# Optimization experiments

Measured on AMD Instinct MI355X. Metric: run time of the kernel, lower is better.

## Reference

```python
import jax, jax.numpy as jnp
import numpy as np

N, F = 1024, 512
H, W = 128, 128
TANX = TANY = 0.5
SCALE_MOD = 1.0


def quat_to_rot(q):
    q = q / jnp.linalg.norm(q, axis=-1, keepdims=True)
    r, x, y, z = q[:, 0], q[:, 1], q[:, 2], q[:, 3]
    R = jnp.stack([
        1 - 2 * (y * y + z * z), 2 * (x * y - r * z), 2 * (x * z + r * y),
        2 * (x * y + r * z), 1 - 2 * (x * x + z * z), 2 * (y * z - r * x),
        2 * (x * z - r * y), 2 * (y * z + r * x), 1 - 2 * (x * x + y * y)], -1)
    return R.reshape(-1, 3, 3)


def setup_inputs() -> dict:
    key = jax.random.key(0)
    ks = jax.random.split(key, 9)
    u = jax.random.uniform(ks[0], (N, 3))
    # place gaussians in front of the camera (z in [2,6], x/y within frustum)
    means3D = jnp.stack([(u[:, 0] - 0.5) * 2.0, (u[:, 1] - 0.5) * 2.0,
                         2.0 + 4.0 * u[:, 2]], axis=1)
    means2D = jnp.zeros((N, 3), jnp.float32)  # grad holder, unused in fwd math
    opacities = 0.05 + 0.9 * jax.random.uniform(ks[1], (N, 1))
    colors_precomp = jax.random.uniform(ks[2], (N, 3))
    semantic_feature = jax.random.uniform(ks[3], (N, F))
    scales = 0.02 + 0.08 * jax.random.uniform(ks[4], (N, 3))
    rotations = jax.random.normal(ks[5], (N, 4))
    viewmatrix = jnp.eye(4, dtype=jnp.float32)
    znear, zfar = 0.01, 100.0
    P = np.zeros((4, 4), np.float32)
    P[0, 0] = 1.0 / TANX
    P[1, 1] = 1.0 / TANY
    P[2, 2] = zfar / (zfar - znear)
    P[2, 3] = -zfar * znear / (zfar - znear)
    P[3, 2] = 1.0
    projmatrix = jnp.asarray(P.T)  # row-vector convention p_h @ M (3DGS style)
    bg = jnp.zeros(3, jnp.float32)
    campos = jnp.zeros(3, jnp.float32)
    conv_w = 0.02 * jax.random.normal(ks[6], (512, F))
    conv_b = 0.01 * jax.random.normal(ks[7], (512,))
    return dict(means3D=means3D, means2D=means2D, opacities=opacities,
                colors_precomp=colors_precomp, semantic_feature=semantic_feature,
                scales=scales, rotations=rotations, viewmatrix=viewmatrix,
                projmatrix=projmatrix, bg=bg, campos=campos,
                conv_w=conv_w, conv_b=conv_b)


def _rasterize(means3D, opacities, colors_precomp, semantic_feature, scales,
               rotations, viewmatrix, projmatrix, bg):
    n = means3D.shape[0]
    ph = jnp.concatenate([means3D, jnp.ones((n, 1), means3D.dtype)], 1)
    p_view = ph @ viewmatrix                     # [N,4] camera space
    p_hom = ph @ projmatrix                      # [N,4] clip space
    p_proj = p_hom[:, :3] / (p_hom[:, 3:4] + 1e-7)
    depth = p_view[:, 2]

    # 3D covariance: Sigma = R S S^T R^T
    R = quat_to_rot(rotations)
    M = R * (scales * SCALE_MOD)[:, None, :]
    cov3D = M @ jnp.swapaxes(M, 1, 2)            # [N,3,3]

    # EWA projection to 2D covariance
    fx, fy = W / (2 * TANX), H / (2 * TANY)
    tz = p_view[:, 2]
    txz = jnp.clip(p_view[:, 0] / tz, -1.3 * TANX, 1.3 * TANX) * tz
    tyz = jnp.clip(p_view[:, 1] / tz, -1.3 * TANY, 1.3 * TANY) * tz
    J = jnp.zeros((n, 2, 3), means3D.dtype)
    J = J.at[:, 0, 0].set(fx / tz).at[:, 0, 2].set(-fx * txz / (tz * tz))
    J = J.at[:, 1, 1].set(fy / tz).at[:, 1, 2].set(-fy * tyz / (tz * tz))
    T = J @ viewmatrix[:3, :3].T[None]           # [N,2,3]
    cov2D = T @ cov3D @ jnp.swapaxes(T, 1, 2)
    cov2D = cov2D.at[:, 0, 0].add(0.3).at[:, 1, 1].add(0.3)  # low-pass dilation

    det = cov2D[:, 0, 0] * cov2D[:, 1, 1] - cov2D[:, 0, 1] ** 2
    det_safe = jnp.where(det == 0, 1.0, det)
    conic = jnp.stack([cov2D[:, 1, 1], -cov2D[:, 0, 1], cov2D[:, 0, 0]], -1) / det_safe[:, None]

    mid = 0.5 * (cov2D[:, 0, 0] + cov2D[:, 1, 1])
    lam1 = mid + jnp.sqrt(jnp.maximum(0.1, mid * mid - det))
    radii = jnp.ceil(3.0 * jnp.sqrt(lam1)).astype(jnp.int32)

    px = ((p_proj[:, 0] + 1.0) * W - 1.0) * 0.5  # ndc2Pix
    py = ((p_proj[:, 1] + 1.0) * H - 1.0) * 0.5
    valid = (depth > 0.2) & (det != 0)
    radii = jnp.where(valid, radii, 0)

    order = jnp.argsort(depth)                   # global front-to-back sort
    gy, gx = jnp.meshgrid(jnp.arange(H, dtype=means3D.dtype),
                          jnp.arange(W, dtype=means3D.dtype), indexing='ij')
    dx = px[order][:, None, None] - gx[None]     # [N,H,W]
    dy = py[order][:, None, None] - gy[None]
    co = conic[order]
    power = (-0.5 * (co[:, 0, None, None] * dx * dx
                     + co[:, 2, None, None] * dy * dy)
             - co[:, 1, None, None] * dx * dy)
    alpha = jnp.minimum(0.99, opacities[order][:, 0, None, None] * jnp.exp(power))
    keep = (power <= 0) & (alpha >= 1.0 / 255.0) & valid[order][:, None, None]
    alpha = jnp.where(keep, alpha, 0.0)

    log1m = jnp.log1p(-alpha)                    # log transmittance increments
    Texcl = jnp.exp(jnp.cumsum(log1m, axis=0) - log1m)  # exclusive cumprod
    w = Texcl * alpha                            # [N,H,W] blend weights
    Tfinal = jnp.exp(jnp.sum(log1m, axis=0))     # [H,W]

    color = jnp.einsum('nhw,nc->chw', w, colors_precomp[order]) \
        + Tfinal[None] * bg[:, None, None]
    feature_map = jnp.einsum('nhw,nf->fhw', w, semantic_feature[order])
    return color, feature_map, radii


def reference(means3D, means2D, opacities, colors_precomp, semantic_feature,
              scales, rotations, viewmatrix, projmatrix, bg, campos,
              conv_w, conv_b):
    color, feature_map, radii = _rasterize(
        means3D, opacities, colors_precomp, semantic_feature, scales,
        rotations, viewmatrix, projmatrix, bg)
    # final 1x1 conv on the rendered feature map
    feature_out = jnp.einsum('fhw,of->ohw', feature_map, conv_w) \
        + conv_b[:, None, None]
    return color, feature_out, radii
```

## Files before the change

kernel.cpp:

```cpp
#include <hip/hip_runtime.h>
#include <hip/hip_bf16.h>
#include <math.h>

#define H_IMG 128
#define W_IMG 128
#define N_G   1024
#define F_DIM 512
#define O_DIM 512
#define PIX   (H_IMG*W_IMG)
#define FEAT_OFF 49152
#define RAD_OFF  (49152 + 512*16384)
#define MAXG  192
#define WT_PITCH 200
#define GT_PITCH 72

typedef __attribute__((ext_vector_type(8))) short bf16x8;
typedef __attribute__((ext_vector_type(4))) float f32x4;

__global__ __launch_bounds__(256) void prep_gemm_kernel(
    const float* __restrict__ means,
    const float* __restrict__ opac,
    const float* __restrict__ colors,
    const float* __restrict__ scales,
    const float* __restrict__ rots,
    const float* __restrict__ view,
    const float* __restrict__ proj,
    const float* __restrict__ S,
    const float* __restrict__ Wm,
    float* __restrict__ psort,
    float* __restrict__ csort,
    float* __restrict__ rb,
    float* __restrict__ radii_out,
    __hip_bfloat16* __restrict__ Gvb)
{
    const int bid = blockIdx.x;
    if (bid >= 16) {
        const int id   = bid - 16;
        const int t    = threadIdx.x;
        const int lane = t & 63;
        const int wv   = t >> 6;
        const int m0   = (id >> 5) * 64 + wv * 16;
        const int o0   = (id & 31) * 16;
        const int lhi  = lane >> 4;
        const int llo  = lane & 15;

        const int arow = m0 + llo;
        const float* Ar = S  + (size_t)arow*F_DIM + 8*lhi;
        const float* Br = Wm + (size_t)(o0 + llo)*F_DIM + 8*lhi;

        f32x4 acc = (f32x4){0.f,0.f,0.f,0.f};

        float4 a0 = *reinterpret_cast<const float4*>(Ar);
        float4 a1 = *reinterpret_cast<const float4*>(Ar + 4);
        float4 b0 = *reinterpret_cast<const float4*>(Br);
        float4 b1 = *reinterpret_cast<const float4*>(Br + 4);

        for (int k0 = 0; k0 < F_DIM; k0 += 32) {
            float4 na0, na1, nb0, nb1;
            const bool more = (k0 + 32) < F_DIM;
            if (more) {
                na0 = *reinterpret_cast<const float4*>(Ar + k0 + 32);
                na1 = *reinterpret_cast<const float4*>(Ar + k0 + 36);
                nb0 = *reinterpret_cast<const float4*>(Br + k0 + 32);
                nb1 = *reinterpret_cast<const float4*>(Br + k0 + 36);
            }
            bf16x8 af, bf;
            af[0]=__bfloat16_as_short(__float2bfloat16(a0.x));
            af[1]=__bfloat16_as_short(__float2bfloat16(a0.y));
            af[2]=__bfloat16_as_short(__float2bfloat16(a0.z));
            af[3]=__bfloat16_as_short(__float2bfloat16(a0.w));
            af[4]=__bfloat16_as_short(__float2bfloat16(a1.x));
            af[5]=__bfloat16_as_short(__float2bfloat16(a1.y));
            af[6]=__bfloat16_as_short(__float2bfloat16(a1.z));
            af[7]=__bfloat16_as_short(__float2bfloat16(a1.w));
            bf[0]=__bfloat16_as_short(__float2bfloat16(b0.x));
            bf[1]=__bfloat16_as_short(__float2bfloat16(b0.y));
            bf[2]=__bfloat16_as_short(__float2bfloat16(b0.z));
            bf[3]=__bfloat16_as_short(__float2bfloat16(b0.w));
            bf[4]=__bfloat16_as_short(__float2bfloat16(b1.x));
            bf[5]=__bfloat16_as_short(__float2bfloat16(b1.y));
            bf[6]=__bfloat16_as_short(__float2bfloat16(b1.z));
            bf[7]=__bfloat16_as_short(__float2bfloat16(b1.w));
            acc = __builtin_amdgcn_mfma_f32_16x16x32_bf16(af, bf, acc, 0, 0, 0);
            if (more) { a0 = na0; a1 = na1; b0 = nb0; b1 = nb1; }
        }

        #pragma unroll
        for (int r = 0; r < 4; ++r) {
            int row = m0 + 4*lhi + r;
            Gvb[(size_t)row*O_DIM + o0 + llo] = __float2bfloat16(acc[r]);
        }
        return;
    }

    __shared__ float d[N_G];
    __shared__ int pr[64][4];
    const int t = threadIdx.x;
    const float v2 = view[2], v6 = view[6], v10 = view[10], v14 = view[14];
    for (int i = t; i < N_G; i += 256)
        d[i] = means[3*i]*v2 + means[3*i+1]*v6 + means[3*i+2]*v10 + v14;
    __syncthreads();

    const int ln = t & 63;
    const int ch = t >> 6;
    const int n  = bid*64 + ln;
    const float depth = d[n];

    {
        int rp = 0;
        const int mbeg = ch*256;
        for (int m = mbeg; m < mbeg + 256; ++m) {
            float dm = d[m];
            rp += (dm < depth) || (dm == depth && m < n);
        }
        pr[ln][ch] = rp;
    }
    __syncthreads();
    if (ch != 0) return;

    const int r = pr[ln][0] + pr[ln][1] + pr[ln][2] + pr[ln][3];

    float x = means[3*n], y = means[3*n+1], z = means[3*n+2];
    float pv0 = x*view[0] + y*view[4] + z*view[8]  + view[12];
    float pv1 = x*view[1] + y*view[5] + z*view[9]  + view[13];
    float ph0 = x*proj[0] + y*proj[4] + z*proj[8]  + proj[12];
    float ph1 = x*proj[1] + y*proj[5] + z*proj[9]  + proj[13];
    float phw = x*proj[3] + y*proj[7] + z*proj[11] + proj[15];
    float denom = phw + 1e-7f;
    float pp0 = ph0/denom, pp1 = ph1/denom;

    float qr=rots[4*n], qx=rots[4*n+1], qy=rots[4*n+2], qz=rots[4*n+3];
    float qn = sqrtf(qr*qr+qx*qx+qy*qy+qz*qz);
    qr/=qn; qx/=qn; qy/=qn; qz/=qn;
    float R00=1.f-2.f*(qy*qy+qz*qz), R01=2.f*(qx*qy-qr*qz), R02=2.f*(qx*qz+qr*qy);
    float R10=2.f*(qx*qy+qr*qz), R11=1.f-2.f*(qx*qx+qz*qz), R12=2.f*(qy*qz-qr*qx);
    float R20=2.f*(qx*qz-qr*qy), R21=2.f*(qy*qz+qr*qx), R22=1.f-2.f*(qx*qx+qy*qy);
    float s0=scales[3*n], s1=scales[3*n+1], s2=scales[3*n+2];
    float M00=R00*s0, M01=R01*s1, M02=R02*s2;
    float M10=R10*s0, M11=R11*s1, M12=R12*s2;
    float M20=R20*s0, M21=R21*s1, M22=R22*s2;
    float c00=M00*M00+M01*M01+M02*M02;
    float c01=M00*M10+M01*M11+M02*M12;
    float c02=M00*M20+M01*M21+M02*M22;
    float c11=M10*M10+M11*M11+M12*M12;
    float c12=M10*M20+M11*M21+M12*M22;
    float c22=M20*M20+M21*M21+M22*M22;

    const float fx=128.f, fy=128.f;
    float tz = depth;
    float txz = fminf(fmaxf(pv0/tz, -0.65f), 0.65f) * tz;
    float tyz = fminf(fmaxf(pv1/tz, -0.65f), 0.65f) * tz;
    float J00 = fx/tz,  J02 = -fx*txz/(tz*tz);
    float J11 = fy/tz,  J12 = -fy*tyz/(tz*tz);
    float T00=J00*view[0] + J02*view[2];
    float T01=J00*view[4] + J02*view[6];
    float T02=J00*view[8] + J02*view[10];
    float T10=J11*view[1] + J12*view[2];
    float T11=J11*view[5] + J12*view[6];
    float T12=J11*view[9] + J12*view[10];
    float u0 = T00*c00 + T01*c01 + T02*c02;
    float u1 = T00*c01 + T01*c11 + T02*c12;
    float u2 = T00*c02 + T01*c12 + T02*c22;
    float v0 = T10*c00 + T11*c01 + T12*c02;
    float v1 = T10*c01 + T11*c11 + T12*c12;
    float v2r= T10*c02 + T11*c12 + T12*c22;
    float a00 = u0*T00 + u1*T01 + u2*T02 + 0.3f;
    float a01 = u0*T10 + u1*T11 + u2*T12;
    float a11 = v0*T10 + v1*T11 + v2r*T12 + 0.3f;

    float det = a00*a11 - a01*a01;
    float dsafe = (det==0.f) ? 1.f : det;
    float inv = 1.f/dsafe;
    float con0 =  a11*inv, con1 = -a01*inv, con2 = a00*inv;
    float mid = 0.5f*(a00+a11);
    float lam1 = mid + sqrtf(fmaxf(0.1f, mid*mid - det));
    int irad = (int)ceilf(3.f*sqrtf(lam1));
    float pxc = ((pp0+1.f)*128.f - 1.f)*0.5f;
    float pyc = ((pp1+1.f)*128.f - 1.f)*0.5f;
    bool valid = (depth > 0.2f) && (det != 0.f);

    radii_out[n] = valid ? (float)irad : 0.f;
    float* p = psort + 8*r;
    p[0]=pxc; p[1]=pyc; p[2]=con0; p[3]=con1; p[4]=con2;
    p[5]=opac[n]; p[6]=(float)n; p[7]= valid ? 1.f : 0.f;
    csort[4*r+0] = colors[3*n+0];
    csort[4*r+1] = colors[3*n+1];
    csort[4*r+2] = colors[3*n+2];
    csort[4*r+3] = 0.f;

    float op = opac[n];
    float tau = logf(255.f * op);
    bool active = valid && (tau > 0.f);
    float rx = active ? (sqrtf(2.f*tau*a00) + 0.01f) : -1.f;
    float ry = active ? (sqrtf(2.f*tau*a11) + 0.01f) : -1.f;
    rb[2*r+0] = rx;
    rb[2*r+1] = ry;
}

__global__ __launch_bounds__(1024) void alphafeat_kernel(
    const float* __restrict__ psort, const float* __restrict__ csort,
    const float* __restrict__ rb, const float* __restrict__ bg,
    const __hip_bfloat16* __restrict__ Gvb, const float* __restrict__ conv_b,
    float* __restrict__ out)
{
    __shared__ __align__(16) char uni[73728];
    float (*pg)[8]       = (float(*)[8])uni;
    float (*cs)[4]       = (float(*)[4])(uni + 32768);
    float (*colbuf)[64][4] = (float(*)[64][4])(uni + 49152);
    float (*Pl)[64]      = (float(*)[64])(uni + 65536);
    short (*GT)[GT_PITCH] = (short(*)[GT_PITCH])uni;

    __shared__ short WT[64][WT_PITCH];
    __shared__ float rbl[N_G][2];
    __shared__ float Tfl[64];
    __shared__ int   idx_lds[MAXG];
    __shared__ int   cntl_s[16];
    __shared__ int   cnt_tot;

    const int t    = threadIdx.x;
    const int c    = t >> 6;
    const int lane = t & 63;
    const int tile = blockIdx.x;
    const int hrow = tile >> 1;
    const int w0   = (tile & 1) * 64;

    {
        float4* pgv = reinterpret_cast<float4*>(&pg[0][0]);
        const float4* ps4 = reinterpret_cast<const float4*>(psort);
        pgv[t]        = ps4[t];
        pgv[t + 1024] = ps4[t + 1024];
        float4* csv = reinterpret_cast<float4*>(&cs[0][0]);
        csv[t] = reinterpret_cast<const float4*>(csort)[t];
        reinterpret_cast<float2*>(&rbl[0][0])[t] =
            reinterpret_cast<const float2*>(rb)[t];
        int* wtz = (int*)&WT[0][0];
        for (int i = t; i < 64*WT_PITCH/2; i += 1024) wtz[i] = 0;
        if (t < MAXG) idx_lds[t] = 0;
    }
    __syncthreads();

    const float gx = (float)(w0 + lane);
    const float gy = (float)hrow;
    const float wlo = (float)w0;
    const float whi = (float)(w0 + 63);

    unsigned long long hitmask;
    {
        int g = c*64 + lane;
        float2 R = *reinterpret_cast<const float2*>(&rbl[g][0]);
        float2 Axy = *reinterpret_cast<const float2*>(&pg[g][0]);
        bool hit = (R.x >= 0.f) && (fabsf(Axy.y - gy) <= R.y)
                && (Axy.x >= wlo - R.x) && (Axy.x <= whi + R.x);
        hitmask = __ballot(hit);
    }

    float pref = 1.f;
    int cnt = 0;
    {
        unsigned long long m = hitmask;
        while (m) {
            int j = (int)__builtin_ctzll(m); m &= m - 1;
            int g = c*64 + j;
            float4 A = *reinterpret_cast<const float4*>(&pg[g][0]);
            float4 B = *reinterpret_cast<const float4*>(&pg[g][4]);
            float dx = A.x - gx, dy = A.y - gy;
            float pw = -0.5f*(A.z*dx*dx + B.x*dy*dy) - A.w*dx*dy;
            float al = fminf(0.99f, B.y*__expf(pw));
            bool keep = (pw <= 0.f) && (al >= (1.f/255.f)) && (B.w > 0.5f);
            float a = keep ? al : 0.f;
            float w = pref * a;
            pref *= 1.f - a;
            cnt += (__ballot(w > 1e-12f) != 0ull) ? 1 : 0;
        }
    }
    Pl[c][lane] = pref;
    if (lane == 0) cntl_s[c] = cnt;
    __syncthreads();

    int base = 0;
    float cp = 1.f;
    for (int cc = 0; cc < c; ++cc) {
        base += cntl_s[cc];
        cp *= Pl[cc][lane];
    }
    if (c == 15) {
        Tfl[lane] = cp * Pl[15][lane];
        if (lane == 0) {
            int tot = base + cntl_s[15];
            cnt_tot = (tot < MAXG) ? tot : MAXG;
        }
    }

    float pref2 = 1.f;
    int slot = base;
    float col0 = 0.f, col1 = 0.f, col2 = 0.f;
    {
        unsigned long long m = hitmask;
        while (m) {
            int j = (int)__builtin_ctzll(m); m &= m - 1;
            int g = c*64 + j;
            float4 A = *reinterpret_cast<const float4*>(&pg[g][0]);
            float4 B = *reinterpret_cast<const float4*>(&pg[g][4]);
            float dx = A.x - gx, dy = A.y - gy;
            float pw = -0.5f*(A.z*dx*dx + B.x*dy*dy) - A.w*dx*dy;
            float al = fminf(0.99f, B.y*__expf(pw));
            bool keep = (pw <= 0.f) && (al >= (1.f/255.f)) && (B.w > 0.5f);
            float a = keep ? al : 0.f;
            float w = pref2 * a;
            pref2 *= 1.f - a;
            if (__ballot(w > 1e-12f) != 0ull) {
                float wfin = w * cp;
                if (slot < MAXG) {
                    WT[lane][slot] = __bfloat16_as_short(__float2bfloat16(wfin));
                    if (lane == 0) idx_lds[slot] = (int)B.z;
                }
                float4 cv = *reinterpret_cast<const float4*>(&cs[g][0]);
                col0 += wfin*cv.x; col1 += wfin*cv.y; col2 += wfin*cv.z;
                ++slot;
            }
        }
    }

    colbuf[c][lane][0] = col0; colbuf[c][lane][1] = col1; colbuf[c][lane][2] = col2;
    __syncthreads();

    if (t < 64) {
        float r = 0.f, g = 0.f, b = 0.f;
        #pragma unroll
        for (int k = 0; k < 16; ++k) {
            r += colbuf[k][t][0]; g += colbuf[k][t][1]; b += colbuf[k][t][2];
        }
        float Tf = Tfl[t];
        int pix = hrow*W_IMG + w0 + t;
        out[0*PIX + pix] = r + Tf*bg[0];
        out[1*PIX + pix] = g + Tf*bg[1];
        out[2*PIX + pix] = b + Tf*bg[2];
    }
    __syncthreads();

    int scnt = cnt_tot;
    scnt = (scnt < 0) ? 0 : ((scnt > MAXG) ? MAXG : scnt);
    const short* gvs = (const short*)Gvb;

    f32x4 acc[2][4];
    #pragma unroll
    for (int i = 0; i < 2; ++i)
        #pragma unroll
        for (int j = 0; j < 4; ++j)
            acc[i][j] = (f32x4){0.f,0.f,0.f,0.f};

    const int nchunk = (scnt + 63) >> 6;
    for (int cc = 0; cc < nchunk; ++cc) {
        const int kbase = cc*64;
        {
            const int o = t & 511;
            const int half = t >> 9;
            #pragma unroll
            for (int b = 0; b < 4; ++b) {
                bf16x8 s;
                #pragma unroll
                for (int j = 0; j < 8; ++j) {
                    int k = kbase + half*32 + b*8 + j;
                    s[j] = (k < scnt) ? gvs[(size_t)idx_lds[k]*O_DIM + o] : (short)0;
                }
                *(bf16x8*)&GT[o][half*32 + b*8] = s;
            }
        }
        __syncthreads();

        #pragma unroll
        for (int ks = 0; ks < 2; ++ks) {
            const int kf = 8*(lane>>4);
            bf16x8 bfr[4];
            #pragma unroll
            for (int pt = 0; pt < 4; ++pt)
                bfr[pt] = *(const bf16x8*)&WT[pt*16 + (lane&15)][kbase + ks*32 + kf];
            #pragma unroll
            for (int ot = 0; ot < 2; ++ot) {
                bf16x8 af = *(const bf16x8*)&GT[c*32 + ot*16 + (lane&15)][ks*32 + kf];
                #pragma unroll
                for (int pt = 0; pt < 4; ++pt)
                    acc[ot][pt] = __builtin_amdgcn_mfma_f32_16x16x32_bf16(
                        af, bfr[pt], acc[ot][pt], 0, 0, 0);
            }
        }
        __syncthreads();
    }

    const int pixbase = hrow*W_IMG + w0;
    #pragma unroll
    for (int ot = 0; ot < 2; ++ot) {
        #pragma unroll
        for (int r = 0; r < 4; ++r) {
            int o = c*32 + ot*16 + 4*(lane>>4) + r;
            float cb = conv_b[o];
            #pragma unroll
            for (int pt = 0; pt < 4; ++pt) {
                out[FEAT_OFF + (size_t)o*PIX + pixbase + pt*16 + (lane&15)]
                    = acc[ot][pt][r] + cb;
            }
        }
    }
}

extern "C" void kernel_launch(void* const* d_in, const int* in_sizes, int n_in,
                              void* d_out, int out_size, void* d_ws, size_t ws_size,
                              hipStream_t stream)
{
    const float* means  = (const float*)d_in[0];
    const float* opac   = (const float*)d_in[2];
    const float* colors = (const float*)d_in[3];
    const float* sem    = (const float*)d_in[4];
    const float* scales = (const float*)d_in[5];
    const float* rots   = (const float*)d_in[6];
    const float* view   = (const float*)d_in[7];
    const float* proj   = (const float*)d_in[8];
    const float* bg     = (const float*)d_in[9];
    const float* conv_w = (const float*)d_in[11];
    const float* conv_b = (const float*)d_in[12];
    float* out = (float*)d_out;

    float* wsf   = (float*)d_ws;
    float* psort = wsf;
    float* csort = wsf + 8192;
    float* rb    = wsf + 13312;
    __hip_bfloat16* Gvb = (__hip_bfloat16*)(wsf + 16384);

    float* radii_out = out + RAD_OFF;

    prep_gemm_kernel<<<528, 256, 0, stream>>>(means, opac, colors, scales,
                                              rots, view, proj, sem, conv_w,
                                              psort, csort, rb, radii_out, Gvb);
    alphafeat_kernel<<<256, 1024, 0, stream>>>(psort, csort, rb, bg, Gvb,
                                               conv_b, out);
}
```

Before: 43.85 us.

## Fuse prep, GEMM and rasterize kernels into one cooperative launch with grid sync

Merges the preprocessing/sort/GEMM kernel and the alpha-blend/feature kernel into a single cooperative kernel of 256 blocks of 1024 threads, separated by a grid-wide sync. The GEMM tiles are redistributed so 8 waves per block each compute one 16x16 tile, and the depth sort runs in the first 16 blocks. This removes one kernel launch and the inter-kernel gap, at the cost of a grid barrier and fewer waves doing the GEMM per block, with a reliance on all 256 large blocks being co-resident.

```diff
diff --git a/kernel.cpp b/kernel.cpp
--- a/kernel.cpp
+++ b/kernel.cpp
@@ -1,6 +1,9 @@
 #include <hip/hip_runtime.h>
 #include <hip/hip_bf16.h>
+#include <hip/hip_cooperative_groups.h>
 #include <math.h>
+
+namespace cg = cooperative_groups;
 
 #define H_IMG 128
 #define W_IMG 128
@@ -17,7 +20,7 @@
 typedef __attribute__((ext_vector_type(8))) short bf16x8;
 typedef __attribute__((ext_vector_type(4))) float f32x4;
 
-__global__ __launch_bounds__(256) void prep_gemm_kernel(
+__global__ __launch_bounds__(1024) void fused_kernel(
     const float* __restrict__ means,
     const float* __restrict__ opac,
     const float* __restrict__ colors,
@@ -31,185 +34,12 @@
     float* __restrict__ csort,
     float* __restrict__ rb,
     float* __restrict__ radii_out,
-    __hip_bfloat16* __restrict__ Gvb)
-{
-    const int bid = blockIdx.x;
-    if (bid >= 16) {
-        const int id   = bid - 16;
-        const int t    = threadIdx.x;
-        const int lane = t & 63;
-        const int wv   = t >> 6;
-        const int m0   = (id >> 5) * 64 + wv * 16;
-        const int o0   = (id & 31) * 16;
-        const int lhi  = lane >> 4;
-        const int llo  = lane & 15;
-
-        const int arow = m0 + llo;
-        const float* Ar = S  + (size_t)arow*F_DIM + 8*lhi;
-        const float* Br = Wm + (size_t)(o0 + llo)*F_DIM + 8*lhi;
-
-        f32x4 acc = (f32x4){0.f,0.f,0.f,0.f};
-
-        float4 a0 = *reinterpret_cast<const float4*>(Ar);
-        float4 a1 = *reinterpret_cast<const float4*>(Ar + 4);
-        float4 b0 = *reinterpret_cast<const float4*>(Br);
-        float4 b1 = *reinterpret_cast<const float4*>(Br + 4);
-
-        for (int k0 = 0; k0 < F_DIM; k0 += 32) {
-            float4 na0, na1, nb0, nb1;
-            const bool more = (k0 + 32) < F_DIM;
-            if (more) {
-                na0 = *reinterpret_cast<const float4*>(Ar + k0 + 32);
-                na1 = *reinterpret_cast<const float4*>(Ar + k0 + 36);
-                nb0 = *reinterpret_cast<const float4*>(Br + k0 + 32);
-                nb1 = *reinterpret_cast<const float4*>(Br + k0 + 36);
-            }
-            bf16x8 af, bf;
-            af[0]=__bfloat16_as_short(__float2bfloat16(a0.x));
-            af[1]=__bfloat16_as_short(__float2bfloat16(a0.y));
-            af[2]=__bfloat16_as_short(__float2bfloat16(a0.z));
-            af[3]=__bfloat16_as_short(__float2bfloat16(a0.w));
-            af[4]=__bfloat16_as_short(__float2bfloat16(a1.x));
-            af[5]=__bfloat16_as_short(__float2bfloat16(a1.y));
-            af[6]=__bfloat16_as_short(__float2bfloat16(a1.z));
-            af[7]=__bfloat16_as_short(__float2bfloat16(a1.w));
-            bf[0]=__bfloat16_as_short(__float2bfloat16(b0.x));
-            bf[1]=__bfloat16_as_short(__float2bfloat16(b0.y));
-            bf[2]=__bfloat16_as_short(__float2bfloat16(b0.z));
-            bf[3]=__bfloat16_as_short(__float2bfloat16(b0.w));
-            bf[4]=__bfloat16_as_short(__float2bfloat16(b1.x));
-            bf[5]=__bfloat16_as_short(__float2bfloat16(b1.y));
-            bf[6]=__bfloat16_as_short(__float2bfloat16(b1.z));
-            bf[7]=__bfloat16_as_short(__float2bfloat16(b1.w));
-            acc = __builtin_amdgcn_mfma_f32_16x16x32_bf16(af, bf, acc, 0, 0, 0);
-            if (more) { a0 = na0; a1 = na1; b0 = nb0; b1 = nb1; }
-        }
-
-        #pragma unroll
-        for (int r = 0; r < 4; ++r) {
-            int row = m0 + 4*lhi + r;
-            Gvb[(size_t)row*O_DIM + o0 + llo] = __float2bfloat16(acc[r]);
-        }
-        return;
-    }
-
-    __shared__ float d[N_G];
-    __shared__ int pr[64][4];
-    const int t = threadIdx.x;
-    const float v2 = view[2], v6 = view[6], v10 = view[10], v14 = view[14];
-    for (int i = t; i < N_G; i += 256)
-        d[i] = means[3*i]*v2 + means[3*i+1]*v6 + means[3*i+2]*v10 + v14;
-    __syncthreads();
-
-    const int ln = t & 63;
-    const int ch = t >> 6;
-    const int n  = bid*64 + ln;
-    const float depth = d[n];
-
-    {
-        int rp = 0;
-        const int mbeg = ch*256;
-        for (int m = mbeg; m < mbeg + 256; ++m) {
-            float dm = d[m];
-            rp += (dm < depth) || (dm == depth && m < n);
-        }
-        pr[ln][ch] = rp;
-    }
-    __syncthreads();
-    if (ch != 0) return;
-
-    const int r = pr[ln][0] + pr[ln][1] + pr[ln][2] + pr[ln][3];
-
-    float x = means[3*n], y = means[3*n+1], z = means[3*n+2];
-    float pv0 = x*view[0] + y*view[4] + z*view[8]  + view[12];
-    float pv1 = x*view[1] + y*view[5] + z*view[9]  + view[13];
-    float ph0 = x*proj[0] + y*proj[4] + z*proj[8]  + proj[12];
-    float ph1 = x*proj[1] + y*proj[5] + z*proj[9]  + proj[13];
-    float phw = x*proj[3] + y*proj[7] + z*proj[11] + proj[15];
-    float denom = phw + 1e-7f;
-    float pp0 = ph0/denom, pp1 = ph1/denom;
-
-    float qr=rots[4*n], qx=rots[4*n+1], qy=rots[4*n+2], qz=rots[4*n+3];
-    float qn = sqrtf(qr*qr+qx*qx+qy*qy+qz*qz);
-    qr/=qn; qx/=qn; qy/=qn; qz/=qn;
-    float R00=1.f-2.f*(qy*qy+qz*qz), R01=2.f*(qx*qy-qr*qz), R02=2.f*(qx*qz+qr*qy);
-    float R10=2.f*(qx*qy+qr*qz), R11=1.f-2.f*(qx*qx+qz*qz), R12=2.f*(qy*qz-qr*qx);
-    float R20=2.f*(qx*qz-qr*qy), R21=2.f*(qy*qz+qr*qx), R22=1.f-2.f*(qx*qx+qy*qy);
-    float s0=scales[3*n], s1=scales[3*n+1], s2=scales[3*n+2];
-    float M00=R00*s0, M01=R01*s1, M02=R02*s2;
-    float M10=R10*s0, M11=R11*s1, M12=R12*s2;
-    float M20=R20*s0, M21=R21*s1, M22=R22*s2;
-    float c00=M00*M00+M01*M01+M02*M02;
-    float c01=M00*M10+M01*M11+M02*M12;
-    float c02=M00*M20+M01*M21+M02*M22;
-    float c11=M10*M10+M11*M11+M12*M12;
-    float c12=M10*M20+M11*M21+M12*M22;
-    float c22=M20*M20+M21*M21+M22*M22;
-
-    const float fx=128.f, fy=128.f;
-    float tz = depth;
-    float txz = fminf(fmaxf(pv0/tz, -0.65f), 0.65f) * tz;
-    float tyz = fminf(fmaxf(pv1/tz, -0.65f), 0.65f) * tz;
-    float J00 = fx/tz,  J02 = -fx*txz/(tz*tz);
-    float J11 = fy/tz,  J12 = -fy*tyz/(tz*tz);
-    float T00=J00*view[0] + J02*view[2];
-    float T01=J00*view[4] + J02*view[6];
-    float T02=J00*view[8] + J02*view[10];
-    float T10=J11*view[1] + J12*view[2];
-    float T11=J11*view[5] + J12*view[6];
-    float T12=J11*view[9] + J12*view[10];
-    float u0 = T00*c00 + T01*c01 + T02*c02;
-    float u1 = T00*c01 + T01*c11 + T02*c12;
-    float u2 = T00*c02 + T01*c12 + T02*c22;
-    float v0 = T10*c00 + T11*c01 + T12*c02;
-    float v1 = T10*c01 + T11*c11 + T12*c12;
-    float v2r= T10*c02 + T11*c12 + T12*c22;
-    float a00 = u0*T00 + u1*T01 + u2*T02 + 0.3f;
-    float a01 = u0*T10 + u1*T11 + u2*T12;
-    float a11 = v0*T10 + v1*T11 + v2r*T12 + 0.3f;
-
-    float det = a00*a11 - a01*a01;
-    float dsafe = (det==0.f) ? 1.f : det;
-    float inv = 1.f/dsafe;
-    float con0 =  a11*inv, con1 = -a01*inv, con2 = a00*inv;
-    float mid = 0.5f*(a00+a11);
-    float lam1 = mid + sqrtf(fmaxf(0.1f, mid*mid - det));
-    int irad = (int)ceilf(3.f*sqrtf(lam1));
-    float pxc = ((pp0+1.f)*128.f - 1.f)*0.5f;
-    float pyc = ((pp1+1.f)*128.f - 1.f)*0.5f;
-    bool valid = (depth > 0.2f) && (det != 0.f);
-
-    radii_out[n] = valid ? (float)irad : 0.f;
-    float* p = psort + 8*r;
-    p[0]=pxc; p[1]=pyc; p[2]=con0; p[3]=con1; p[4]=con2;
-    p[5]=opac[n]; p[6]=(float)n; p[7]= valid ? 1.f : 0.f;
-    csort[4*r+0] = colors[3*n+0];
-    csort[4*r+1] = colors[3*n+1];
-    csort[4*r+2] = colors[3*n+2];
-    csort[4*r+3] = 0.f;
-
-    float op = opac[n];
-    float tau = logf(255.f * op);
-    bool active = valid && (tau > 0.f);
-    float rx = active ? (sqrtf(2.f*tau*a00) + 0.01f) : -1.f;
-    float ry = active ? (sqrtf(2.f*tau*a11) + 0.01f) : -1.f;
-    rb[2*r+0] = rx;
-    rb[2*r+1] = ry;
-}
-
-__global__ __launch_bounds__(1024) void alphafeat_kernel(
-    const float* __restrict__ psort, const float* __restrict__ csort,
-    const float* __restrict__ rb, const float* __restrict__ bg,
-    const __hip_bfloat16* __restrict__ Gvb, const float* __restrict__ conv_b,
+    __hip_bfloat16* __restrict__ Gvb,
+    const float* __restrict__ bg,
+    const float* __restrict__ conv_b,
     float* __restrict__ out)
 {
     __shared__ __align__(16) char uni[73728];
-    float (*pg)[8]       = (float(*)[8])uni;
-    float (*cs)[4]       = (float(*)[4])(uni + 32768);
-    float (*colbuf)[64][4] = (float(*)[64][4])(uni + 49152);
-    float (*Pl)[64]      = (float(*)[64])(uni + 65536);
-    short (*GT)[GT_PITCH] = (short(*)[GT_PITCH])uni;
-
     __shared__ short WT[64][WT_PITCH];
     __shared__ float rbl[N_G][2];
     __shared__ float Tfl[64];
@@ -217,10 +47,182 @@
     __shared__ int   cntl_s[16];
     __shared__ int   cnt_tot;
 
+    const int bid  = blockIdx.x;
     const int t    = threadIdx.x;
+    const int lane = t & 63;
+
+    if (bid < 16) {
+        float* d  = (float*)uni;
+        int*   pr = (int*)(uni + 4096);
+        const float v2 = view[2], v6 = view[6], v10 = view[10], v14 = view[14];
+        if (t < N_G)
+            d[t] = means[3*t]*v2 + means[3*t+1]*v6 + means[3*t+2]*v10 + v14;
+        __syncthreads();
+
+        if (t < 256) {
+            const int ln = t & 63;
+            const int ch = t >> 6;
+            const int n  = bid*64 + ln;
+            const float depth = d[n];
+            int rp = 0;
+            const int mbeg = ch*256;
+            for (int m = mbeg; m < mbeg + 256; ++m) {
+                float dm = d[m];
+                rp += (dm < depth) || (dm == depth && m < n);
+            }
+            pr[ln*4 + ch] = rp;
+        }
+        __syncthreads();
+
+        if (t < 64) {
+            const int n = bid*64 + t;
+            const float depth = d[n];
+            const int r = pr[t*4+0] + pr[t*4+1] + pr[t*4+2] + pr[t*4+3];
+
+            float x = means[3*n], y = means[3*n+1], z = means[3*n+2];
+            float pv0 = x*view[0] + y*view[4] + z*view[8]  + view[12];
+            float pv1 = x*view[1] + y*view[5] + z*view[9]  + view[13];
+            float ph0 = x*proj[0] + y*proj[4] + z*proj[8]  + proj[12];
+            float ph1 = x*proj[1] + y*proj[5] + z*proj[9]  + proj[13];
+            float phw = x*proj[3] + y*proj[7] + z*proj[11] + proj[15];
+            float denom = phw + 1e-7f;
+            float pp0 = ph0/denom, pp1 = ph1/denom;
+
+            float qr=rots[4*n], qx=rots[4*n+1], qy=rots[4*n+2], qz=rots[4*n+3];
+            float qn = sqrtf(qr*qr+qx*qx+qy*qy+qz*qz);
+            qr/=qn; qx/=qn; qy/=qn; qz/=qn;
+            float R00=1.f-2.f*(qy*qy+qz*qz), R01=2.f*(qx*qy-qr*qz), R02=2.f*(qx*qz+qr*qy);
+            float R10=2.f*(qx*qy+qr*qz), R11=1.f-2.f*(qx*qx+qz*qz), R12=2.f*(qy*qz-qr*qx);
+            float R20=2.f*(qx*qz-qr*qy), R21=2.f*(qy*qz+qr*qx), R22=1.f-2.f*(qx*qx+qy*qy);
+            float s0=scales[3*n], s1=scales[3*n+1], s2=scales[3*n+2];
+            float M00=R00*s0, M01=R01*s1, M02=R02*s2;
+            float M10=R10*s0, M11=R11*s1, M12=R12*s2;
+            float M20=R20*s0, M21=R21*s1, M22=R22*s2;
+            float c00=M00*M00+M01*M01+M02*M02;
+            float c01=M00*M10+M01*M11+M02*M12;
+            float c02=M00*M20+M01*M21+M02*M22;
+            float c11=M10*M10+M11*M11+M12*M12;
+            float c12=M10*M20+M11*M21+M12*M22;
+            float c22=M20*M20+M21*M21+M22*M22;
+
+            const float fx=128.f, fy=128.f;
+            float tz = depth;
+            float txz = fminf(fmaxf(pv0/tz, -0.65f), 0.65f) * tz;
+            float tyz = fminf(fmaxf(pv1/tz, -0.65f), 0.65f) * tz;
+            float J00 = fx/tz,  J02 = -fx*txz/(tz*tz);
+            float J11 = fy/tz,  J12 = -fy*tyz/(tz*tz);
+            float T00=J00*view[0] + J02*view[2];
+            float T01=J00*view[4] + J02*view[6];
+            float T02=J00*view[8] + J02*view[10];
+            float T10=J11*view[1] + J12*view[2];
+            float T11=J11*view[5] + J12*view[6];
+            float T12=J11*view[9] + J12*view[10];
+            float u0 = T00*c00 + T01*c01 + T02*c02;
+            float u1 = T00*c01 + T01*c11 + T02*c12;
+            float u2 = T00*c02 + T01*c12 + T02*c22;
+            float v0 = T10*c00 + T11*c01 + T12*c02;
+            float v1 = T10*c01 + T11*c11 + T12*c12;
+            float v2r= T10*c02 + T11*c12 + T12*c22;
+            float a00 = u0*T00 + u1*T01 + u2*T02 + 0.3f;
+            float a01 = u0*T10 + u1*T11 + u2*T12;
+            float a11 = v0*T10 + v1*T11 + v2r*T12 + 0.3f;
+
+            float det = a00*a11 - a01*a01;
+            float dsafe = (det==0.f) ? 1.f : det;
+            float inv = 1.f/dsafe;
+            float con0 =  a11*inv, con1 = -a01*inv, con2 = a00*inv;
+            float mid = 0.5f*(a00+a11);
+            float lam1 = mid + sqrtf(fmaxf(0.1f, mid*mid - det));
+            int irad = (int)ceilf(3.f*sqrtf(lam1));
+            float pxc = ((pp0+1.f)*128.f - 1.f)*0.5f;
+            float pyc = ((pp1+1.f)*128.f - 1.f)*0.5f;
+            bool valid = (depth > 0.2f) && (det != 0.f);
+
+            radii_out[n] = valid ? (float)irad : 0.f;
+            float* p = psort + 8*r;
+            p[0]=pxc; p[1]=pyc; p[2]=con0; p[3]=con1; p[4]=con2;
+            p[5]=opac[n]; p[6]=(float)n; p[7]= valid ? 1.f : 0.f;
+            csort[4*r+0] = colors[3*n+0];
+            csort[4*r+1] = colors[3*n+1];
+            csort[4*r+2] = colors[3*n+2];
+            csort[4*r+3] = 0.f;
+
+            float op = opac[n];
+            float tau = logf(255.f * op);
+            bool active = valid && (tau > 0.f);
+            rb[2*r+0] = active ? (sqrtf(2.f*tau*a00) + 0.01f) : -1.f;
+            rb[2*r+1] = active ? (sqrtf(2.f*tau*a11) + 0.01f) : -1.f;
+        }
+    }
+
+    {
+        const int wv = t >> 6;
+        if (wv < 8) {
+            const int tile_id = bid*8 + wv;
+            const int m0  = (tile_id >> 5) * 16;
+            const int o0  = (tile_id & 31) * 16;
+            const int lhi = lane >> 4;
+            const int llo = lane & 15;
+
+            const int arow = m0 + llo;
+            const float* Ar = S  + (size_t)arow*F_DIM + 8*lhi;
+            const float* Br = Wm + (size_t)(o0 + llo)*F_DIM + 8*lhi;
+
+            f32x4 acc = (f32x4){0.f,0.f,0.f,0.f};
+
+            float4 a0 = *reinterpret_cast<const float4*>(Ar);
+            float4 a1 = *reinterpret_cast<const float4*>(Ar + 4);
+            float4 b0 = *reinterpret_cast<const float4*>(Br);
+            float4 b1 = *reinterpret_cast<const float4*>(Br + 4);
+
+            for (int k0 = 0; k0 < F_DIM; k0 += 32) {
+                float4 na0, na1, nb0, nb1;
+                const bool more = (k0 + 32) < F_DIM;
+                if (more) {
+                    na0 = *reinterpret_cast<const float4*>(Ar + k0 + 32);
+                    na1 = *reinterpret_cast<const float4*>(Ar + k0 + 36);
+                    nb0 = *reinterpret_cast<const float4*>(Br + k0 + 32);
+                    nb1 = *reinterpret_cast<const float4*>(Br + k0 + 36);
+                }
+                bf16x8 af, bf;
+                af[0]=__bfloat16_as_short(__float2bfloat16(a0.x));
+                af[1]=__bfloat16_as_short(__float2bfloat16(a0.y));
+                af[2]=__bfloat16_as_short(__float2bfloat16(a0.z));
+                af[3]=__bfloat16_as_short(__float2bfloat16(a0.w));
+                af[4]=__bfloat16_as_short(__float2bfloat16(a1.x));
+                af[5]=__bfloat16_as_short(__float2bfloat16(a1.y));
+                af[6]=__bfloat16_as_short(__float2bfloat16(a1.z));
+                af[7]=__bfloat16_as_short(__float2bfloat16(a1.w));
+                bf[0]=__bfloat16_as_short(__float2bfloat16(b0.x));
+                bf[1]=__bfloat16_as_short(__float2bfloat16(b0.y));
+                bf[2]=__bfloat16_as_short(__float2bfloat16(b0.z));
+                bf[3]=__bfloat16_as_short(__float2bfloat16(b0.w));
+                bf[4]=__bfloat16_as_short(__float2bfloat16(b1.x));
+                bf[5]=__bfloat16_as_short(__float2bfloat16(b1.y));
+                bf[6]=__bfloat16_as_short(__float2bfloat16(b1.z));
+                bf[7]=__bfloat16_as_short(__float2bfloat16(b1.w));
+                acc = __builtin_amdgcn_mfma_f32_16x16x32_bf16(af, bf, acc, 0, 0, 0);
+                if (more) { a0 = na0; a1 = na1; b0 = nb0; b1 = nb1; }
+            }
+
+            #pragma unroll
+            for (int r = 0; r < 4; ++r) {
+                int row = m0 + 4*lhi + r;
+                Gvb[(size_t)row*O_DIM + o0 + llo] = __float2bfloat16(acc[r]);
+            }
+        }
+    }
+
+    cg::this_grid().sync();
+
+    float (*pg)[8]       = (float(*)[8])uni;
+    float (*cs)[4]       = (float(*)[4])(uni + 32768);
+    float (*colbuf)[64][4] = (float(*)[64][4])(uni + 49152);
+    float (*Pl)[64]      = (float(*)[64])(uni + 65536);
+    short (*GT)[GT_PITCH] = (short(*)[GT_PITCH])uni;
+
     const int c    = t >> 6;
-    const int lane = t & 63;
-    const int tile = blockIdx.x;
+    const int tile = bid;
     const int hrow = tile >> 1;
     const int w0   = (tile & 1) * 64;
 
@@ -428,9 +430,12 @@
 
     float* radii_out = out + RAD_OFF;
 
-    prep_gemm_kernel<<<528, 256, 0, stream>>>(means, opac, colors, scales,
-                                              rots, view, proj, sem, conv_w,
-                                              psort, csort, rb, radii_out, Gvb);
-    alphafeat_kernel<<<256, 1024, 0, stream>>>(psort, csort, rb, bg, Gvb,
-                                               conv_b, out);
+    void* args[] = {
+        (void*)&means, (void*)&opac, (void*)&colors, (void*)&scales,
+        (void*)&rots, (void*)&view, (void*)&proj, (void*)&sem, (void*)&conv_w,
+        (void*)&psort, (void*)&csort, (void*)&rb, (void*)&radii_out,
+        (void*)&Gvb, (void*)&bg, (void*)&conv_b, (void*)&out
+    };
+    hipLaunchCooperativeKernel((const void*)fused_kernel, dim3(256), dim3(1024),
+                               args, 0, stream);
 }
```

Result: slower. 82.17 us (+87.4%).
